# Optimization experiments

Measured on AMD Instinct MI355X. Metric: run time of the kernel, lower is better.

Reference implementation:

```python
import jax, jax.numpy as jnp
import numpy as np

N = 16384
E = 524288
IN_DIM = 512
HID = 256
NCLS = 64


def setup_inputs() -> dict:
    key = jax.random.key(0)
    k1, k2, k3, k4, k5, k6 = jax.random.split(key, 6)
    X = jax.random.normal(k1, (N, IN_DIM), dtype=jnp.float32)
    edge_index = jax.random.randint(k2, (2, E), 0, N, dtype=jnp.int64)
    # torch nn.Linear params: y = x @ W.T + b
    W1 = jax.random.normal(k3, (HID, IN_DIM), dtype=jnp.float32) * (1.0 / np.sqrt(IN_DIM))
    b1 = jax.random.normal(k4, (HID,), dtype=jnp.float32) * 0.01
    W2 = jax.random.normal(k5, (NCLS, HID), dtype=jnp.float32) * (1.0 / np.sqrt(HID))
    b2 = jax.random.normal(k6, (NCLS,), dtype=jnp.float32) * 0.01
    return {"X": X, "edge_index": edge_index, "W1": W1, "b1": b1, "W2": W2, "b2": b2}


def _build_a_hat(edge_index, n):
    # Dense adjacency via scatter-set, exactly as the torch code does.
    A = jnp.zeros((n, n), dtype=jnp.float32)
    A = A.at[edge_index[0], edge_index[1]].set(1.0)
    A = A + A.T
    A = (A > 0).astype(jnp.float32)
    A = A + jnp.eye(n, dtype=jnp.float32)
    # symmetric normalization: D^-1/2 A D^-1/2 (diag matmuls == broadcast)
    deg = A.sum(axis=1)
    dis = jnp.power(deg + 1e-8, -0.5)
    return dis[:, None] * A * dis[None, :]


def reference(X, edge_index, W1, b1, W2, b2):
    n = X.shape[0]
    A_hat = _build_a_hat(edge_index, n)
    H = A_hat @ X                      # [N, in_dim]
    H = H @ W1.T + b1                  # lin1
    H = jax.nn.relu(H)
    # dropout is identity in eval mode
    H = A_hat @ H                      # [N, hidden]
    H = H @ W2.T + b2                  # lin2 -> [N, num_classes]
    return H
```

## Files before the change

### kernel.cpp

```cpp
#include <hip/hip_runtime.h>
#include <stdint.h>

#define N_NODES 16384
#define N_EDGES 524288
#define IN_DIM  512
#define HID     256
#define NCLS    64
#define LSTRIDE 192
#define NBKT    1024
#define BCAP    1536
#define GEMM_BLKS 512

typedef __bf16 bf16x8 __attribute__((ext_vector_type(8)));
typedef float  f32x4  __attribute__((ext_vector_type(4)));

__device__ __forceinline__ unsigned short f2bf(float f) {
    unsigned int u = __float_as_uint(f);
    u += 0x7FFFu + ((u >> 16) & 1u);
    return (unsigned short)(u >> 16);
}
__device__ __forceinline__ float bflo(unsigned int u) { return __uint_as_float(u << 16); }
__device__ __forceinline__ float bfhi(unsigned int u) { return __uint_as_float(u & 0xFFFF0000u); }

__global__ __launch_bounds__(256) void bucket_edges(
    const void* __restrict__ ep, unsigned int* __restrict__ gcnt,
    unsigned int* __restrict__ gbuf) {
    __shared__ int sflag;
    __shared__ unsigned int lcnt[NBKT];
    __shared__ unsigned int lbase[NBKT];
    const int tid = threadIdx.x;
    if (tid == 0) {
        const int* p = (const int*)ep;
        int odd = 1;
        for (int k = 0; k < 64; ++k)
            if (p[2 * k + 1] != 0) odd = 0;
        sflag = odd;
    }
    for (int b = tid; b < NBKT; b += 256) lcnt[b] = 0;
    __syncthreads();

    const int e0 = blockIdx.x * 2048 + tid;
    int s[8], d[8];
    if (sflag) {
        const long long* p = (const long long*)ep;
        #pragma unroll
        for (int q = 0; q < 8; ++q) {
            s[q] = (int)p[e0 + q * 256];
            d[q] = (int)p[N_EDGES + e0 + q * 256];
        }
    } else {
        const int* p = (const int*)ep;
        #pragma unroll
        for (int q = 0; q < 8; ++q) {
            s[q] = p[e0 + q * 256];
            d[q] = p[N_EDGES + e0 + q * 256];
        }
    }
    unsigned int meta[16];
    #pragma unroll
    for (int q = 0; q < 8; ++q) {
        int b0 = s[q] >> 4, b1 = d[q] >> 4;
        unsigned int sl0 = atomicAdd(&lcnt[b0], 1u);
        unsigned int sl1 = atomicAdd(&lcnt[b1], 1u);
        meta[2 * q]     = (unsigned int)b0 | (sl0 << 10);
        meta[2 * q + 1] = (unsigned int)b1 | (sl1 << 10);
    }
    __syncthreads();
    for (int b = tid; b < NBKT; b += 256) {
        unsigned int c = lcnt[b];
        lbase[b] = c ? atomicAdd(&gcnt[b], c) : 0u;
    }
    __syncthreads();
    #pragma unroll
    for (int q = 0; q < 8; ++q) {
        unsigned int m0 = meta[2 * q];
        unsigned int bk0 = m0 & 1023u;
        unsigned int sl0 = lbase[bk0] + (m0 >> 10);
        if (sl0 < BCAP)
            gbuf[(size_t)bk0 * BCAP + sl0] =
                ((unsigned int)(s[q] & 15) << 14) | (unsigned int)d[q];
        unsigned int m1 = meta[2 * q + 1];
        unsigned int bk1 = m1 & 1023u;
        unsigned int sl1 = lbase[bk1] + (m1 >> 10);
        if (sl1 < BCAP)
            gbuf[(size_t)bk1 * BCAP + sl1] =
                ((unsigned int)(d[q] & 15) << 14) | (unsigned int)s[q];
    }
}

__device__ __forceinline__ void csr_body(
    int bkt, const unsigned int* __restrict__ gcnt,
    const unsigned int* __restrict__ gbuf, float* __restrict__ dis,
    int* __restrict__ ncnt, unsigned short* __restrict__ lists, char* smem) {
    unsigned int* bml = (unsigned int*)smem;
    const int tid = threadIdx.x;
    const int node0 = bkt * 16;
    #pragma unroll
    for (int q = 0; q < 32; ++q) bml[tid + q * 256] = 0;
    __syncthreads();
    const unsigned int n = min(gcnt[bkt], (unsigned int)BCAP);
    for (unsigned int l = tid; l < n; l += 256) {
        unsigned int e = gbuf[(size_t)bkt * BCAP + l];
        unsigned int local = e >> 14, nbr = e & 16383u;
        atomicOr(&bml[local * 512 + (nbr >> 5)], 1u << (nbr & 31u));
    }
    __syncthreads();
    const int wid = tid >> 6, lane = tid & 63;
    for (int nn = wid; nn < 16; nn += 4) {
        const int node = node0 + nn;
        const unsigned int* row = bml + nn * 512 + lane * 8;
        unsigned int w[8];
        int c = 0;
        #pragma unroll
        for (int j = 0; j < 8; ++j) { w[j] = row[j]; c += __popc(w[j]); }
        int inc = c;
        #pragma unroll
        for (int dd = 1; dd < 64; dd <<= 1) {
            int t = __shfl_up(inc, dd);
            if (lane >= dd) inc += t;
        }
        int total = __shfl(inc, 63);
        unsigned short* dst = lists + (size_t)node * LSTRIDE + (inc - c);
        int k = 0;
        #pragma unroll
        for (int j = 0; j < 8; ++j) {
            unsigned int bits = w[j];
            int base = (lane * 8 + j) * 32;
            while (bits) {
                int b = __ffs(bits) - 1;
                bits &= bits - 1;
                dst[k++] = (unsigned short)(base + b);
            }
        }
        if (lane == 63) {
            lists[(size_t)node * LSTRIDE + total] = (unsigned short)node;
            ncnt[node] = total + 1;
            dis[node] = 1.0f / sqrtf((float)(total + 1) + 1e-8f);
        }
    }
}

template <bool F32>
__device__ __forceinline__ uint4 ld_chunk(const void* __restrict__ G,
                                          size_t row, int KD, int k0, int s) {
    if constexpr (F32) {
        const float* g = (const float*)G + row * KD + k0 + s * 8;
        float4 v0 = *(const float4*)g;
        float4 v1 = *(const float4*)(g + 4);
        uint4 w;
        w.x = (unsigned int)f2bf(v0.x) | ((unsigned int)f2bf(v0.y) << 16);
        w.y = (unsigned int)f2bf(v0.z) | ((unsigned int)f2bf(v0.w) << 16);
        w.z = (unsigned int)f2bf(v1.x) | ((unsigned int)f2bf(v1.y) << 16);
        w.w = (unsigned int)f2bf(v1.z) | ((unsigned int)f2bf(v1.w) << 16);
        return w;
    } else {
        return *(const uint4*)((const unsigned short*)G + row * KD + k0 + s * 8);
    }
}

template <int BM, int BN, int KD, int ND, bool AF32, bool BF32>
__device__ __forceinline__ void gemm_body(
    int bx, int by, const void* __restrict__ Ag, const void* __restrict__ Bg,
    unsigned short* __restrict__ Cg, const float* __restrict__ dis, char* smem) {
    constexpr int FM = BM / 32, FN = BN / 32;
    constexpr int NK = KD / 64;
    unsigned short* Asm = (unsigned short*)smem;
    unsigned short* Bsm = (unsigned short*)smem + BM * 64;
    const int tid = threadIdx.x;
    const int lane = tid & 63;
    const int wid = tid >> 6;
    const int wm = wid >> 1, wn = wid & 1;
    const int m0 = bx * BM, n0 = by * BN;

    uint4 ra[BM / 32], rb[BN / 32];
    #pragma unroll
    for (int q = 0; q < BM / 32; ++q) {
        int cch = tid + 256 * q, r = cch >> 3, s = cch & 7;
        ra[q] = ld_chunk<AF32>(Ag, (size_t)(m0 + r), KD, 0, s);
    }
    #pragma unroll
    for (int q = 0; q < BN / 32; ++q) {
        int cch = tid + 256 * q, r = cch >> 3, s = cch & 7;
        rb[q] = ld_chunk<BF32>(Bg, (size_t)(n0 + r), KD, 0, s);
    }

    f32x4 acc[FM][FN] = {};

    for (int kt = 0; kt < NK; ++kt) {
        __syncthreads();
        #pragma unroll
        for (int q = 0; q < BM / 32; ++q) {
            int cch = tid + 256 * q, r = cch >> 3, s = cch & 7;
            *(uint4*)((char*)Asm + r * 128 + ((s ^ (r & 7)) << 4)) = ra[q];
        }
        #pragma unroll
        for (int q = 0; q < BN / 32; ++q) {
            int cch = tid + 256 * q, r = cch >> 3, s = cch & 7;
            *(uint4*)((char*)Bsm + r * 128 + ((s ^ (r & 7)) << 4)) = rb[q];
        }
        __syncthreads();
        if (kt + 1 < NK) {
            int k0 = (kt + 1) * 64;
            #pragma unroll
            for (int q = 0; q < BM / 32; ++q) {
                int cch = tid + 256 * q, r = cch >> 3, s = cch & 7;
                ra[q] = ld_chunk<AF32>(Ag, (size_t)(m0 + r), KD, k0, s);
            }
            #pragma unroll
            for (int q = 0; q < BN / 32; ++q) {
                int cch = tid + 256 * q, r = cch >> 3, s = cch & 7;
                rb[q] = ld_chunk<BF32>(Bg, (size_t)(n0 + r), KD, k0, s);
            }
        }
        #pragma unroll
        for (int ks = 0; ks < 2; ++ks) {
            bf16x8 af[FM], bg[FN];
            #pragma unroll
            for (int i = 0; i < FM; ++i) {
                int row = wm * (BM / 2) + i * 16 + (lane & 15);
                int slot = (ks * 4 + (lane >> 4)) ^ (row & 7);
                af[i] = *(const bf16x8*)((const char*)Asm + row * 128 + slot * 16);
            }
            #pragma unroll
            for (int j = 0; j < FN; ++j) {
                int row = wn * (BN / 2) + j * 16 + (lane & 15);
                int slot = (ks * 4 + (lane >> 4)) ^ (row & 7);
                bg[j] = *(const bf16x8*)((const char*)Bsm + row * 128 + slot * 16);
            }
            #pragma unroll
            for (int i = 0; i < FM; ++i)
                #pragma unroll
                for (int j = 0; j < FN; ++j)
                    acc[i][j] = __builtin_amdgcn_mfma_f32_16x16x32_bf16(af[i], bg[j], acc[i][j], 0, 0, 0);
        }
    }

    #pragma unroll
    for (int i = 0; i < FM; ++i) {
        #pragma unroll
        for (int e = 0; e < 4; ++e) {
            int row = m0 + wm * (BM / 2) + i * 16 + ((lane >> 4) << 2) + e;
            float dm = dis ? dis[row] : 1.0f;
            #pragma unroll
            for (int j = 0; j < FN; ++j) {
                int col = n0 + wn * (BN / 2) + j * 16 + (lane & 15);
                Cg[(size_t)row * ND + col] = f2bf(acc[i][j][e] * dm);
            }
        }
    }
}

__global__ __launch_bounds__(256) void csr_gemm(
    const float* __restrict__ X, const float* __restrict__ W1,
    unsigned short* __restrict__ Y, const unsigned int* __restrict__ gcnt,
    const unsigned int* __restrict__ gbuf, float* __restrict__ dis,
    int* __restrict__ ncnt, unsigned short* __restrict__ lists) {
    __shared__ __align__(16) char smem[32768];
    if (blockIdx.x < GEMM_BLKS) {
        int gb = blockIdx.x;
        gemm_body<64, 128, IN_DIM, HID, true, true>(
            gb & 255, gb >> 8, X, W1, Y, nullptr, smem);
    } else {
        csr_body(blockIdx.x - GEMM_BLKS, gcnt, gbuf, dis, ncnt, lists, smem);
    }
}

__global__ __launch_bounds__(256) void gemm2_k(
    const unsigned short* __restrict__ H1, const float* __restrict__ W2,
    unsigned short* __restrict__ Z, const float* __restrict__ dis) {
    __shared__ __align__(16) char smem[(64 + 64) * 64 * 2];
    gemm_body<64, 64, HID, NCLS, false, true>(blockIdx.x, 0, H1, W2, Z, dis, smem);
}

__global__ __launch_bounds__(256) void spmm_hid(
    const int* __restrict__ ncnt, const unsigned short* __restrict__ lists,
    const float* __restrict__ dis, const unsigned short* __restrict__ Yp,
    const float* __restrict__ bias, unsigned int* __restrict__ H1b) {
    const int bid = blockIdx.x;
    const int r = bid & 7;
    const int fh = r >> 2;
    const int wid = threadIdx.x >> 6, lane = threadIdx.x & 63;
    const int i = (bid >> 3) * 16 + (r & 3) * 4 + wid;

    __shared__ unsigned int sl[4][LSTRIDE];
    __shared__ float dl[4][LSTRIDE];
    const int n = min(ncnt[i], LSTRIDE);
    for (int l = lane; l < n; l += 64) {
        int j = lists[(size_t)i * LSTRIDE + l];
        sl[wid][l] = (unsigned int)j << 9;
        dl[wid][l] = dis[j];
    }
    __syncthreads();

    const int hw = lane >> 5, p = lane & 31;
    const char* Ybase = (const char*)Yp + fh * 256 + p * 8;
    float a0 = 0, a1 = 0, a2 = 0, a3 = 0;
    float b0 = 0, b1 = 0, b2 = 0, b3 = 0;
    float c0 = 0, c1 = 0, c2 = 0, c3 = 0;
    float d0 = 0, d1 = 0, d2 = 0, d3 = 0;
    int l = 0;
    for (; l + 8 <= n; l += 8) {
        int i0 = l + hw, i1 = l + 2 + hw, i2 = l + 4 + hw, i3 = l + 6 + hw;
        uint2 u0 = *(const uint2*)(Ybase + sl[wid][i0]);
        uint2 u1 = *(const uint2*)(Ybase + sl[wid][i1]);
        uint2 u2 = *(const uint2*)(Ybase + sl[wid][i2]);
        uint2 u3 = *(const uint2*)(Ybase + sl[wid][i3]);
        float w0 = dl[wid][i0], w1 = dl[wid][i1], w2 = dl[wid][i2], w3 = dl[wid][i3];
        a0 = fmaf(w0, bflo(u0.x), a0); a1 = fmaf(w0, bfhi(u0.x), a1);
        a2 = fmaf(w0, bflo(u0.y), a2); a3 = fmaf(w0, bfhi(u0.y), a3);
        b0 = fmaf(w1, bflo(u1.x), b0); b1 = fmaf(w1, bfhi(u1.x), b1);
        b2 = fmaf(w1, bflo(u1.y), b2); b3 = fmaf(w1, bfhi(u1.y), b3);
        c0 = fmaf(w2, bflo(u2.x), c0); c1 = fmaf(w2, bfhi(u2.x), c1);
        c2 = fmaf(w2, bflo(u2.y), c2); c3 = fmaf(w2, bfhi(u2.y), c3);
        d0 = fmaf(w3, bflo(u3.x), d0); d1 = fmaf(w3, bfhi(u3.x), d1);
        d2 = fmaf(w3, bflo(u3.y), d2); d3 = fmaf(w3, bfhi(u3.y), d3);
    }
    for (; l + hw < n; l += 2) {
        int i0 = l + hw;
        uint2 u = *(const uint2*)(Ybase + sl[wid][i0]);
        float w = dl[wid][i0];
        a0 = fmaf(w, bflo(u.x), a0); a1 = fmaf(w, bfhi(u.x), a1);
        a2 = fmaf(w, bflo(u.y), a2); a3 = fmaf(w, bfhi(u.y), a3);
    }
    a0 += (b0 + c0) + d0; a1 += (b1 + c1) + d1;
    a2 += (b2 + c2) + d2; a3 += (b3 + c3) + d3;
    a0 += __shfl_xor(a0, 32);
    a1 += __shfl_xor(a1, 32);
    a2 += __shfl_xor(a2, 32);
    a3 += __shfl_xor(a3, 32);
    if (hw == 0) {
        float di = dis[i];
        float4 bb = *(const float4*)&bias[fh * 128 + 4 * p];
        float v0 = fmaxf(fmaf(di, a0, bb.x), 0.0f);
        float v1 = fmaxf(fmaf(di, a1, bb.y), 0.0f);
        float v2 = fmaxf(fmaf(di, a2, bb.z), 0.0f);
        float v3 = fmaxf(fmaf(di, a3, bb.w), 0.0f);
        unsigned int olo = (unsigned int)f2bf(v0) | ((unsigned int)f2bf(v1) << 16);
        unsigned int ohi = (unsigned int)f2bf(v2) | ((unsigned int)f2bf(v3) << 16);
        unsigned int* op = &H1b[(size_t)i * 128 + fh * 64 + 2 * p];
        __builtin_nontemporal_store(olo, op);
        __builtin_nontemporal_store(ohi, op + 1);
    }
}

__global__ __launch_bounds__(256) void spmm_out(
    const int* __restrict__ ncnt, const unsigned short* __restrict__ lists,
    const float* __restrict__ dis, const unsigned short* __restrict__ Zp,
    const float* __restrict__ bias, float* __restrict__ out) {
    const int wid = threadIdx.x >> 6, lane = threadIdx.x & 63;
    const int i = blockIdx.x * 4 + wid;
    __shared__ unsigned int sl[4][LSTRIDE];
    const int n = min(ncnt[i], LSTRIDE);
    for (int l = lane; l < n; l += 64)
        sl[wid][l] = (unsigned int)lists[(size_t)i * LSTRIDE + l] << 7;
    __syncthreads();

    const int hw = lane >> 5, p = lane & 31;
    const char* Zbase = (const char*)Zp + p * 4;
    float s0 = 0, s1 = 0, t0 = 0, t1 = 0, q0 = 0, q1 = 0, r0 = 0, r1 = 0;
    int l = 0;
    for (; l + 8 <= n; l += 8) {
        unsigned int ua = *(const unsigned int*)(Zbase + sl[wid][l + hw]);
        unsigned int ub = *(const unsigned int*)(Zbase + sl[wid][l + 2 + hw]);
        unsigned int uc = *(const unsigned int*)(Zbase + sl[wid][l + 4 + hw]);
        unsigned int ud = *(const unsigned int*)(Zbase + sl[wid][l + 6 + hw]);
        s0 += bflo(ua); s1 += bfhi(ua);
        t0 += bflo(ub); t1 += bfhi(ub);
        q0 += bflo(uc); q1 += bfhi(uc);
        r0 += bflo(ud); r1 += bfhi(ud);
    }
    for (; l + hw < n; l += 2) {
        unsigned int u = *(const unsigned int*)(Zbase + sl[wid][l + hw]);
        s0 += bflo(u); s1 += bfhi(u);
    }
    s0 += (t0 + q0) + r0; s1 += (t1 + q1) + r1;
    s0 += __shfl_xor(s0, 32);
    s1 += __shfl_xor(s1, 32);
    if (hw == 0) {
        float di = dis[i];
        __builtin_nontemporal_store(fmaf(di, s0, bias[2 * p]), &out[(size_t)i * 64 + 2 * p]);
        __builtin_nontemporal_store(fmaf(di, s1, bias[2 * p + 1]), &out[(size_t)i * 64 + 2 * p + 1]);
    }
}

extern "C" void kernel_launch(void* const* d_in, const int* in_sizes, int n_in,
                              void* d_out, int out_size, void* d_ws, size_t ws_size,
                              hipStream_t stream) {
    const float* X  = (const float*)d_in[0];
    const void*  EI = d_in[1];
    const float* W1 = (const float*)d_in[2];
    const float* b1 = (const float*)d_in[3];
    const float* W2 = (const float*)d_in[4];
    const float* b2 = (const float*)d_in[5];
    float* out = (float*)d_out;

    char* ws = (char*)d_ws;
    char* p = ws;
    unsigned int* gcnt = (unsigned int*)p;       p += 8192;
    unsigned int* gbuf = (unsigned int*)p;       p += (size_t)NBKT * BCAP * 4;
    float* dis = (float*)p;                      p += (size_t)N_NODES * 4;
    int* ncnt = (int*)p;                         p += (size_t)N_NODES * 4;
    unsigned short* lists = (unsigned short*)p;  p += (size_t)N_NODES * LSTRIDE * 2;
    unsigned short* Y   = (unsigned short*)p;    p += (size_t)N_NODES * HID * 2;
    unsigned int* H1b   = (unsigned int*)p;      p += (size_t)N_NODES * HID * 2;
    unsigned short* Z   = (unsigned short*)p;    p += (size_t)N_NODES * NCLS * 2;

    hipMemsetAsync(gcnt, 0, NBKT * 4, stream);
    bucket_edges<<<N_EDGES / 2048, 256, 0, stream>>>(EI, gcnt, gbuf);
    csr_gemm<<<GEMM_BLKS + NBKT, 256, 0, stream>>>(X, W1, Y, gcnt, gbuf,
                                                   dis, ncnt, lists);
    spmm_hid<<<2 * N_NODES / 4, 256, 0, stream>>>(ncnt, lists, dis, Y, b1, H1b);
    gemm2_k<<<N_NODES / 64, 256, 0, stream>>>((const unsigned short*)H1b, W2, Z, dis);
    spmm_out<<<N_NODES / 4, 256, 0, stream>>>(ncnt, lists, dis, Z, b2, out);
}
```

Measured before the change: 115.7 us.

## Fuse edge bucketing into GEMM1 launch with per-block slices, drop global atomics

```diff
diff --git a/kernel.cpp b/kernel.cpp
--- a/kernel.cpp
+++ b/kernel.cpp
@@ -8,7 +8,8 @@
 #define NCLS    64
 #define LSTRIDE 192
 #define NBKT    1024
-#define BCAP    1536
+#define SCAP    24
+#define NBBLK   256
 #define GEMM_BLKS 512
 
 typedef __bf16 bf16x8 __attribute__((ext_vector_type(8)));
@@ -22,12 +23,11 @@
 __device__ __forceinline__ float bflo(unsigned int u) { return __uint_as_float(u << 16); }
 __device__ __forceinline__ float bfhi(unsigned int u) { return __uint_as_float(u & 0xFFFF0000u); }
 
-__global__ __launch_bounds__(256) void bucket_edges(
-    const void* __restrict__ ep, unsigned int* __restrict__ gcnt,
-    unsigned int* __restrict__ gbuf) {
+__device__ __forceinline__ void bucket_body(
+    int blk, const void* __restrict__ ep, unsigned int* __restrict__ cnt,
+    unsigned int* __restrict__ gbuf, char* smem) {
+    unsigned int* lcnt = (unsigned int*)smem;
     __shared__ int sflag;
-    __shared__ unsigned int lcnt[NBKT];
-    __shared__ unsigned int lbase[NBKT];
     const int tid = threadIdx.x;
     if (tid == 0) {
         const int* p = (const int*)ep;
@@ -39,7 +39,7 @@
     for (int b = tid; b < NBKT; b += 256) lcnt[b] = 0;
     __syncthreads();
 
-    const int e0 = blockIdx.x * 2048 + tid;
+    const int e0 = blk * 2048 + tid;
     int s[8], d[8];
     if (sflag) {
         const long long* p = (const long long*)ep;
@@ -56,53 +56,44 @@
             d[q] = p[N_EDGES + e0 + q * 256];
         }
     }
-    unsigned int meta[16];
+    unsigned int* myslice = gbuf + (size_t)blk * NBKT * SCAP;
     #pragma unroll
     for (int q = 0; q < 8; ++q) {
         int b0 = s[q] >> 4, b1 = d[q] >> 4;
         unsigned int sl0 = atomicAdd(&lcnt[b0], 1u);
         unsigned int sl1 = atomicAdd(&lcnt[b1], 1u);
-        meta[2 * q]     = (unsigned int)b0 | (sl0 << 10);
-        meta[2 * q + 1] = (unsigned int)b1 | (sl1 << 10);
-    }
-    __syncthreads();
-    for (int b = tid; b < NBKT; b += 256) {
-        unsigned int c = lcnt[b];
-        lbase[b] = c ? atomicAdd(&gcnt[b], c) : 0u;
-    }
-    __syncthreads();
-    #pragma unroll
-    for (int q = 0; q < 8; ++q) {
-        unsigned int m0 = meta[2 * q];
-        unsigned int bk0 = m0 & 1023u;
-        unsigned int sl0 = lbase[bk0] + (m0 >> 10);
-        if (sl0 < BCAP)
-            gbuf[(size_t)bk0 * BCAP + sl0] =
+        if (sl0 < SCAP)
+            myslice[b0 * SCAP + sl0] =
                 ((unsigned int)(s[q] & 15) << 14) | (unsigned int)d[q];
-        unsigned int m1 = meta[2 * q + 1];
-        unsigned int bk1 = m1 & 1023u;
-        unsigned int sl1 = lbase[bk1] + (m1 >> 10);
-        if (sl1 < BCAP)
-            gbuf[(size_t)bk1 * BCAP + sl1] =
+        if (sl1 < SCAP)
+            myslice[b1 * SCAP + sl1] =
                 ((unsigned int)(d[q] & 15) << 14) | (unsigned int)s[q];
     }
-}
-
-__device__ __forceinline__ void csr_body(
-    int bkt, const unsigned int* __restrict__ gcnt,
-    const unsigned int* __restrict__ gbuf, float* __restrict__ dis,
-    int* __restrict__ ncnt, unsigned short* __restrict__ lists, char* smem) {
-    unsigned int* bml = (unsigned int*)smem;
+    __syncthreads();
+    unsigned int* mycnt = cnt + (size_t)blk * NBKT;
+    for (int b = tid; b < NBKT; b += 256)
+        mycnt[b] = min(lcnt[b], (unsigned int)SCAP);
+}
+
+__global__ __launch_bounds__(256) void build_csr(
+    const unsigned int* __restrict__ cnt, const unsigned int* __restrict__ gbuf,
+    float* __restrict__ dis, int* __restrict__ ncnt,
+    unsigned short* __restrict__ lists) {
+    __shared__ unsigned int bml[16 * 512];
     const int tid = threadIdx.x;
+    const int bkt = blockIdx.x;
     const int node0 = bkt * 16;
     #pragma unroll
     for (int q = 0; q < 32; ++q) bml[tid + q * 256] = 0;
     __syncthreads();
-    const unsigned int n = min(gcnt[bkt], (unsigned int)BCAP);
-    for (unsigned int l = tid; l < n; l += 256) {
-        unsigned int e = gbuf[(size_t)bkt * BCAP + l];
-        unsigned int local = e >> 14, nbr = e & 16383u;
-        atomicOr(&bml[local * 512 + (nbr >> 5)], 1u << (nbr & 31u));
+    {
+        const unsigned int c = cnt[(size_t)tid * NBKT + bkt];
+        const unsigned int* sp = gbuf + ((size_t)tid * NBKT + bkt) * SCAP;
+        for (unsigned int l = 0; l < c; ++l) {
+            unsigned int e = sp[l];
+            unsigned int local = e >> 14, nbr = e & 16383u;
+            atomicOr(&bml[local * 512 + (nbr >> 5)], 1u << (nbr & 31u));
+        }
     }
     __syncthreads();
     const int wid = tid >> 6, lane = tid & 63;
@@ -250,26 +241,25 @@
     }
 }
 
-__global__ __launch_bounds__(256) void csr_gemm(
+__global__ __launch_bounds__(256) void bucket_gemm(
     const float* __restrict__ X, const float* __restrict__ W1,
-    unsigned short* __restrict__ Y, const unsigned int* __restrict__ gcnt,
-    const unsigned int* __restrict__ gbuf, float* __restrict__ dis,
-    int* __restrict__ ncnt, unsigned short* __restrict__ lists) {
-    __shared__ __align__(16) char smem[32768];
+    unsigned short* __restrict__ Y, const void* __restrict__ ep,
+    unsigned int* __restrict__ cnt, unsigned int* __restrict__ gbuf) {
+    __shared__ __align__(16) char smem[(64 + 128) * 64 * 2];
     if (blockIdx.x < GEMM_BLKS) {
         int gb = blockIdx.x;
         gemm_body<64, 128, IN_DIM, HID, true, true>(
             gb & 255, gb >> 8, X, W1, Y, nullptr, smem);
     } else {
-        csr_body(blockIdx.x - GEMM_BLKS, gcnt, gbuf, dis, ncnt, lists, smem);
+        bucket_body(blockIdx.x - GEMM_BLKS, ep, cnt, gbuf, smem);
     }
 }
 
 __global__ __launch_bounds__(256) void gemm2_k(
     const unsigned short* __restrict__ H1, const float* __restrict__ W2,
     unsigned short* __restrict__ Z, const float* __restrict__ dis) {
-    __shared__ __align__(16) char smem[(64 + 64) * 64 * 2];
-    gemm_body<64, 64, HID, NCLS, false, true>(blockIdx.x, 0, H1, W2, Z, dis, smem);
+    __shared__ __align__(16) char smem[(128 + 64) * 64 * 2];
+    gemm_body<128, 64, HID, NCLS, false, true>(blockIdx.x, 0, H1, W2, Z, dis, smem);
 }
 
 __global__ __launch_bounds__(256) void spmm_hid(
@@ -396,8 +386,8 @@
 
     char* ws = (char*)d_ws;
     char* p = ws;
-    unsigned int* gcnt = (unsigned int*)p;       p += 8192;
-    unsigned int* gbuf = (unsigned int*)p;       p += (size_t)NBKT * BCAP * 4;
+    unsigned int* cnt  = (unsigned int*)p;       p += (size_t)NBBLK * NBKT * 4;
+    unsigned int* gbuf = (unsigned int*)p;       p += (size_t)NBBLK * NBKT * SCAP * 4;
     float* dis = (float*)p;                      p += (size_t)N_NODES * 4;
     int* ncnt = (int*)p;                         p += (size_t)N_NODES * 4;
     unsigned short* lists = (unsigned short*)p;  p += (size_t)N_NODES * LSTRIDE * 2;
@@ -405,11 +395,9 @@
     unsigned int* H1b   = (unsigned int*)p;      p += (size_t)N_NODES * HID * 2;
     unsigned short* Z   = (unsigned short*)p;    p += (size_t)N_NODES * NCLS * 2;
 
-    hipMemsetAsync(gcnt, 0, NBKT * 4, stream);
-    bucket_edges<<<N_EDGES / 2048, 256, 0, stream>>>(EI, gcnt, gbuf);
-    csr_gemm<<<GEMM_BLKS + NBKT, 256, 0, stream>>>(X, W1, Y, gcnt, gbuf,
-                                                   dis, ncnt, lists);
+    bucket_gemm<<<GEMM_BLKS + NBBLK, 256, 0, stream>>>(X, W1, Y, EI, cnt, gbuf);
+    build_csr<<<NBKT, 256, 0, stream>>>(cnt, gbuf, dis, ncnt, lists);
     spmm_hid<<<2 * N_NODES / 4, 256, 0, stream>>>(ncnt, lists, dis, Y, b1, H1b);
-    gemm2_k<<<N_NODES / 64, 256, 0, stream>>>((const unsigned short*)H1b, W2, Z, dis);
+    gemm2_k<<<N_NODES / 128, 256, 0, stream>>>((const unsigned short*)H1b, W2, Z, dis);
     spmm_out<<<N_NODES / 4, 256, 0, stream>>>(ncnt, lists, dis, Z, b2, out);
 }
```

Measured after the change: 115.2 us. No clear change (-0.5%).
